# Kernel optimization log

Measured on AMD Instinct MI355X. Metric: run time of the kernel, lower is better.

The kernel has to match this reference:

```python
import jax, jax.numpy as jnp
import numpy as np

DIM = 768
D_STATE = 16
D_INNER = 2 * DIM  # expand=2


def setup_inputs() -> dict:
    key = jax.random.key(0)
    k_x, k_in, k_conv, k_out = jax.random.split(key, 4)
    B, L = 1, 4096
    x = jax.random.normal(k_x, (B, L, DIM), dtype=jnp.float32)
    # torch Linear weight layout: [out_features, in_features]
    W_in = jax.random.normal(k_in, (3 * D_INNER + 2 * D_STATE, DIM), dtype=jnp.float32) * 0.02
    # depthwise conv1d kernel: [out_ch=d_inner, in_ch/groups=1, k=3]
    W_conv = jax.random.normal(k_conv, (D_INNER, 1, 3), dtype=jnp.float32) * 0.1
    W_out = jax.random.normal(k_out, (DIM, D_INNER), dtype=jnp.float32) * 0.02
    A_log = jnp.log(jnp.tile(jnp.arange(1, D_STATE + 1, dtype=jnp.float32), (D_INNER, 1)))
    D = jnp.ones((D_INNER,), dtype=jnp.float32)
    return {"x": x, "W_in": W_in, "W_conv": W_conv, "W_out": W_out, "A_log": A_log, "D": D}


def reference(x, W_in, W_conv, W_out, A_log, D):
    d_inner = W_conv.shape[0]
    d_state = A_log.shape[1]
    Bsz = x.shape[0]

    xz = x @ W_in.T  # [B, L, 3*d_inner + 2*d_state]
    x_inner, z, B_ssm, C_ssm, delta = jnp.split(
        xz, [d_inner, 2 * d_inner, 2 * d_inner + d_state, 2 * d_inner + 2 * d_state], axis=-1
    )

    # depthwise conv over sequence: [B, d_inner, L]
    xc = jax.lax.conv_general_dilated(
        x_inner.transpose(0, 2, 1), W_conv,
        window_strides=(1,), padding=[(1, 1)], feature_group_count=d_inner,
    ).transpose(0, 2, 1)  # back to [B, L, d_inner]
    xc = jax.nn.silu(xc)

    A = -jnp.exp(A_log)  # [d_inner, d_state]
    delta = jax.nn.softplus(delta)  # [B, L, d_inner]
    dA = jnp.exp(jnp.einsum('bld,dn->bldn', delta, A))           # [B, L, d_inner, d_state]
    dBx = jnp.einsum('bld,bln,bld->bldn', delta, B_ssm, xc)      # delta_B * x fused

    def step(h, inp):
        da_t, dbx_t, c_t = inp  # [B,d,n], [B,d,n], [B,n]
        h = da_t * h + dbx_t
        y_t = jnp.einsum('bdn,bn->bd', h, c_t)
        return h, y_t

    h0 = jnp.zeros((Bsz, d_inner, d_state), dtype=x.dtype)
    _, ys = jax.lax.scan(
        step, h0,
        (dA.transpose(1, 0, 2, 3), dBx.transpose(1, 0, 2, 3), C_ssm.transpose(1, 0, 2)),
    )  # ys: [L, B, d_inner]

    y = ys.transpose(1, 0, 2) + xc * D  # skip connection
    y = y * jax.nn.silu(z)
    return y @ W_out.T  # [B, L, dim]
```

## Files before the change

### kernel.cpp

```cpp
#include <hip/hip_runtime.h>
#include <hip/hip_bf16.h>
#include <math.h>

#define LSEQ   4096
#define DIM    768
#define DINNER 1536
#define DSTATE 16
#define NCOLS  4640
#define NCH    128
#define CLEN   32
#define NPAD   4736
#define DXW    1568

typedef _Float16 f16;
typedef __attribute__((ext_vector_type(8))) _Float16 f16x8;
typedef __attribute__((ext_vector_type(4))) float f32x4;

__device__ __forceinline__ void gld_lds16(void* lds_dst, const void* gsrc) {
    __builtin_amdgcn_global_load_lds(
        (__attribute__((address_space(1))) void*)(gsrc),
        (__attribute__((address_space(3))) void*)(lds_dst), 16, 0, 0);
}

#define G1K    768
#define G1_NT  12
#define G1_BM  256
#define G1_BN  128
#define G1_RT  384
#define G1_LDSE (G1_RT * 64)

__global__ __launch_bounds__(512) void gemm1_pipe(const f16* __restrict__ A,
                                                  const f16* __restrict__ B,
                                                  float* __restrict__ C,
                                                  f16* __restrict__ Xb,
                                                  f16* __restrict__ Zb) {
    __shared__ __align__(16) f16 S[3 * G1_LDSE];

    const int P   = gridDim.x >> 3;
    const int idx = (blockIdx.x & 7) * P + (blockIdx.x >> 3);
    const int m0  = (idx & 15) * G1_BM;
    const int n0  = (idx >> 4) * G1_BN;

    const int tid  = threadIdx.x;
    const int w    = tid >> 6;
    const int lane = tid & 63;
    const int wr   = w >> 1;
    const int wc   = w & 1;
    const int m    = lane & 15;
    const int q    = lane >> 4;
    const int rl8  = lane >> 3;
    const int bsel = lane & 7;

    const f16* gb[6];
#pragma unroll
    for (int s = 0; s < 6; ++s) {
        const int rl  = (w + 8 * s) * 8 + rl8;
        const int blk = bsel ^ (rl & 7);
        gb[s] = (rl < G1_BM) ? A + (size_t)(m0 + rl) * G1K + blk * 8
                             : B + (size_t)(n0 + rl - G1_BM) * G1K + blk * 8;
    }

    f32x4 acc[4][4];
#pragma unroll
    for (int i = 0; i < 4; i++)
#pragma unroll
        for (int j = 0; j < 4; j++) acc[i][j] = (f32x4){0.f, 0.f, 0.f, 0.f};

    auto stg2 = [&](int kt, int s0) {
        f16* dst = S + (kt % 3) * G1_LDSE;
#pragma unroll
        for (int s = s0; s < s0 + 2; ++s)
            gld_lds16(dst + (w + 8 * s) * 512, gb[s] + kt * 64);
    };
    auto stg6 = [&](int kt) {
        f16* dst = S + (kt % 3) * G1_LDSE;
#pragma unroll
        for (int s = 0; s < 6; ++s)
            gld_lds16(dst + (w + 8 * s) * 512, gb[s] + kt * 64);
    };

    stg6(0);
    stg6(1);

#pragma unroll
    for (int kt = 0; kt < G1_NT; ++kt) {
        if (kt < G1_NT - 1) asm volatile("s_waitcnt vmcnt(6)" ::: "memory");
        else                asm volatile("s_waitcnt vmcnt(0)" ::: "memory");
        __builtin_amdgcn_s_barrier();
        const f16* As = S + (kt % 3) * G1_LDSE;
        const f16* Bs = As + G1_BM * 64;
        const bool pf = (kt + 2 < G1_NT);

        f16x8 af0[2][2], af2[2][2], bh0[2][2], bh2[2][2];

#pragma unroll
        for (int kk = 0; kk < 2; ++kk) {
            const int fo = (((q + 4 * kk) ^ (m & 7)) << 3);
#pragma unroll
            for (int i = 0; i < 2; ++i) {
                af0[kk][i] = *(const f16x8*)&As[(wr * 64 + i * 16 + m) * 64 + fo];
                bh0[kk][i] = *(const f16x8*)&Bs[(wc * 64 + i * 16 + m) * 64 + fo];
            }
        }
        if (pf) stg2(kt + 2, 0);
        __builtin_amdgcn_s_barrier();
        asm volatile("s_waitcnt lgkmcnt(0)" ::: "memory");
        __builtin_amdgcn_sched_barrier(0);
        __builtin_amdgcn_s_setprio(1);
#pragma unroll
        for (int kk = 0; kk < 2; ++kk)
#pragma unroll
            for (int i = 0; i < 2; ++i)
#pragma unroll
                for (int j = 0; j < 2; ++j)
                    acc[i][j] = __builtin_amdgcn_mfma_f32_16x16x32_f16(
                        af0[kk][i], bh0[kk][j], acc[i][j], 0, 0, 0);
        __builtin_amdgcn_s_setprio(0);

#pragma unroll
        for (int kk = 0; kk < 2; ++kk) {
            const int fo = (((q + 4 * kk) ^ (m & 7)) << 3);
#pragma unroll
            for (int j = 0; j < 2; ++j)
                bh2[kk][j] = *(const f16x8*)&Bs[(wc * 64 + (j + 2) * 16 + m) * 64 + fo];
        }
        if (pf) stg2(kt + 2, 2);
        __builtin_amdgcn_s_barrier();
        asm volatile("s_waitcnt lgkmcnt(0)" ::: "memory");
        __builtin_amdgcn_sched_barrier(0);
        __builtin_amdgcn_s_setprio(1);
#pragma unroll
        for (int kk = 0; kk < 2; ++kk)
#pragma unroll
            for (int i = 0; i < 2; ++i)
#pragma unroll
                for (int j = 0; j < 2; ++j)
                    acc[i][j + 2] = __builtin_amdgcn_mfma_f32_16x16x32_f16(
                        af0[kk][i], bh2[kk][j], acc[i][j + 2], 0, 0, 0);
        __builtin_amdgcn_s_setprio(0);

#pragma unroll
        for (int kk = 0; kk < 2; ++kk) {
            const int fo = (((q + 4 * kk) ^ (m & 7)) << 3);
#pragma unroll
            for (int i = 0; i < 2; ++i)
                af2[kk][i] = *(const f16x8*)&As[(wr * 64 + (i + 2) * 16 + m) * 64 + fo];
        }
        if (pf) stg2(kt + 2, 4);
        __builtin_amdgcn_s_barrier();
        asm volatile("s_waitcnt lgkmcnt(0)" ::: "memory");
        __builtin_amdgcn_sched_barrier(0);
        __builtin_amdgcn_s_setprio(1);
#pragma unroll
        for (int kk = 0; kk < 2; ++kk)
#pragma unroll
            for (int i = 0; i < 2; ++i)
#pragma unroll
                for (int j = 0; j < 2; ++j)
                    acc[i + 2][j] = __builtin_amdgcn_mfma_f32_16x16x32_f16(
                        af2[kk][i], bh0[kk][j], acc[i + 2][j], 0, 0, 0);
        __builtin_amdgcn_s_setprio(0);

        __builtin_amdgcn_s_setprio(1);
#pragma unroll
        for (int kk = 0; kk < 2; ++kk)
#pragma unroll
            for (int i = 0; i < 2; ++i)
#pragma unroll
                for (int j = 0; j < 2; ++j)
                    acc[i + 2][j + 2] = __builtin_amdgcn_mfma_f32_16x16x32_f16(
                        af2[kk][i], bh2[kk][j], acc[i + 2][j + 2], 0, 0, 0);
        __builtin_amdgcn_s_setprio(0);
    }

    if (n0 < DINNER) {
#pragma unroll
        for (int i = 0; i < 4; i++)
#pragma unroll
            for (int j = 0; j < 4; j++) {
                const int col  = n0 + wc * 64 + j * 16 + m;
                const int rowb = m0 + wr * 64 + i * 16 + q * 4;
#pragma unroll
                for (int r = 0; r < 4; r++)
                    Xb[(size_t)(rowb + r) * DINNER + col] = (f16)acc[i][j][r];
            }
        return;
    }
    if (n0 < 2 * DINNER) {
#pragma unroll
        for (int i = 0; i < 4; i++)
#pragma unroll
            for (int j = 0; j < 4; j++) {
                const int col  = n0 - DINNER + wc * 64 + j * 16 + m;
                const int rowb = m0 + wr * 64 + i * 16 + q * 4;
#pragma unroll
                for (int r = 0; r < 4; r++)
                    Zb[(size_t)(rowb + r) * DINNER + col] = (f16)acc[i][j][r];
            }
        return;
    }
#pragma unroll
    for (int i = 0; i < 4; i++)
#pragma unroll
        for (int j = 0; j < 4; j++) {
            const int col = n0 - 2 * DINNER + wc * 64 + j * 16 + m;
            if (col >= DXW) continue;
            const int rowb = m0 + wr * 64 + i * 16 + q * 4;
#pragma unroll
            for (int r = 0; r < 4; r++)
                C[(size_t)(rowb + r) * DXW + col] = acc[i][j][r];
        }
}

template<int BM, int BN, int WM, int WN, int NTB, bool COLM, bool ZMODE>
__global__ __launch_bounds__(256) void gemm_f16(const f16* __restrict__ A,
                                                const f16* __restrict__ B,
                                                float* __restrict__ C,
                                                f16* __restrict__ Xb,
                                                f16* __restrict__ Zb,
                                                int M, int N, int K, int ldc) {
    constexpr int MI  = WM / 16;
    constexpr int NI  = WN / 16;
    constexpr int NWN = BN / WN;
    constexpr int RT  = BM + BN;
    constexpr int NS  = RT / 8;

    __shared__ __align__(16) f16 S[RT * 64];
    f16* As = S;
    f16* Bs = S + BM * 64;

    const int P   = gridDim.x >> 3;
    const int idx = (blockIdx.x & 7) * P + (blockIdx.x >> 3);
    const int m0  = (COLM ? (idx % NTB) : (idx / NTB)) * BM;
    const int n0  = (COLM ? (idx / NTB) : (idx % NTB)) * BN;

    const int tid  = threadIdx.x;
    const int w    = tid >> 6;
    const int lane = tid & 63;
    const int wr   = w / NWN;
    const int wc   = w % NWN;
    const int m    = lane & 15;
    const int q    = lane >> 4;
    const int rl8  = lane >> 3;
    const int bsel = lane & 7;

    f32x4 acc[MI][NI];
#pragma unroll
    for (int i = 0; i < MI; i++)
#pragma unroll
        for (int j = 0; j < NI; j++) acc[i][j] = (f32x4){0.f, 0.f, 0.f, 0.f};

    for (int k0 = 0; k0 < K; k0 += 64) {
#pragma unroll
        for (int t = w; t < NS; t += 4) {
            const int rl  = t * 8 + rl8;
            const int blk = bsel ^ (rl & 7);
            const f16* g = (rl < BM)
                ? A + (size_t)(m0 + rl) * K + k0 + blk * 8
                : B + (size_t)(n0 + rl - BM) * K + k0 + blk * 8;
            gld_lds16(S + t * 8 * 64, g);
        }
        __syncthreads();

#pragma unroll
        for (int kk = 0; kk < 2; kk++) {
            const int fo = (((q + 4 * kk) ^ (m & 7)) << 3);
            f16x8 af[MI], bh[NI];
#pragma unroll
            for (int i = 0; i < MI; i++)
                af[i] = *(const f16x8*)&As[(wr * WM + i * 16 + m) * 64 + fo];
#pragma unroll
            for (int j = 0; j < NI; j++)
                bh[j] = *(const f16x8*)&Bs[(wc * WN + j * 16 + m) * 64 + fo];
#pragma unroll
            for (int i = 0; i < MI; i++)
#pragma unroll
                for (int j = 0; j < NI; j++)
                    acc[i][j] = __builtin_amdgcn_mfma_f32_16x16x32_f16(
                        af[i], bh[j], acc[i][j], 0, 0, 0);
        }
        __syncthreads();
    }

    if (ZMODE && n0 < DINNER) {
#pragma unroll
        for (int i = 0; i < MI; i++)
#pragma unroll
            for (int j = 0; j < NI; j++) {
                const int col  = n0 + wc * WN + j * 16 + m;
                const int rowb = m0 + wr * WM + i * 16 + q * 4;
#pragma unroll
                for (int r = 0; r < 4; r++)
                    Xb[(size_t)(rowb + r) * DINNER + col] = (f16)acc[i][j][r];
            }
        return;
    }
    if (ZMODE && n0 < 2 * DINNER) {
#pragma unroll
        for (int i = 0; i < MI; i++)
#pragma unroll
            for (int j = 0; j < NI; j++) {
                const int col  = n0 - DINNER + wc * WN + j * 16 + m;
                const int rowb = m0 + wr * WM + i * 16 + q * 4;
#pragma unroll
                for (int r = 0; r < 4; r++)
                    Zb[(size_t)(rowb + r) * DINNER + col] = (f16)acc[i][j][r];
            }
        return;
    }
#pragma unroll
    for (int i = 0; i < MI; i++)
#pragma unroll
        for (int j = 0; j < NI; j++) {
            const int col  = (ZMODE ? n0 - 2 * DINNER : n0) + wc * WN + j * 16 + m;
            const int lim  = ZMODE ? DXW : N;
            if (col >= lim) continue;
            const int rowb = m0 + wr * WM + i * 16 + q * 4;
#pragma unroll
            for (int r = 0; r < 4; r++)
                C[(size_t)(rowb + r) * ldc + col] = acc[i][j][r];
        }
}

#define E0 (LSEQ * DIM)
#define E1 (E0 + NPAD * DIM)
#define E2 (E1 + DIM * DINNER)

__global__ __launch_bounds__(256) void cvt_all(const float* __restrict__ x,
                                               const float* __restrict__ Wi,
                                               const float* __restrict__ Wo,
                                               f16* __restrict__ Ax,
                                               f16* __restrict__ Bw,
                                               f16* __restrict__ Bo) {
    int i = (blockIdx.x * 256 + threadIdx.x) * 4;
    if (i < E0) {
        float4 v = *(const float4*)(x + i);
        Ax[i] = (f16)v.x; Ax[i+1] = (f16)v.y; Ax[i+2] = (f16)v.z; Ax[i+3] = (f16)v.w;
    } else if (i < E1) {
        int e = i - E0;
        int n = e / DIM;
        if (n < NCOLS) {
            float4 v = *(const float4*)(Wi + e);
            Bw[e] = (f16)v.x; Bw[e+1] = (f16)v.y; Bw[e+2] = (f16)v.z; Bw[e+3] = (f16)v.w;
        } else {
            Bw[e] = (f16)0.f; Bw[e+1] = (f16)0.f; Bw[e+2] = (f16)0.f; Bw[e+3] = (f16)0.f;
        }
    } else if (i < E2) {
        int e = i - E1;
        float4 v = *(const float4*)(Wo + e);
        Bo[e] = (f16)v.x; Bo[e+1] = (f16)v.y; Bo[e+2] = (f16)v.z; Bo[e+3] = (f16)v.w;
    }
}

__global__ __launch_bounds__(256) void scan1_kernel(const float* __restrict__ Dxz,
                                                    const f16* __restrict__ Xb,
                                                    const float* __restrict__ Wc,
                                                    const float* __restrict__ A_log,
                                                    float* __restrict__ aprod,
                                                    float* __restrict__ hend) {
    __shared__ float Bs[CLEN * DSTATE];
    const int d  = blockIdx.x * 256 + threadIdx.x;
    const int c  = blockIdx.y;
    const int l0 = c * CLEN;
    for (int i = threadIdx.x; i < CLEN * DSTATE; i += 256)
        Bs[i] = Dxz[(size_t)(l0 + (i >> 4)) * DXW + (i & 15)];
    float Areg[DSTATE];
#pragma unroll
    for (int n = 0; n < DSTATE; n++) Areg[n] = -__expf(A_log[d * DSTATE + n]);
    const float w0 = Wc[d * 3 + 0], w1 = Wc[d * 3 + 1], w2 = Wc[d * 3 + 2];
    float xm = (l0 > 0) ? (float)Xb[(size_t)(l0 - 1) * DINNER + d] : 0.f;
    float x0 = (float)Xb[(size_t)l0 * DINNER + d];
    float ld_xp   = (float)Xb[(size_t)(l0 + 1) * DINNER + d];
    float ld_draw = Dxz[(size_t)l0 * DXW + 32 + d];
    __syncthreads();

    float h[DSTATE];
#pragma unroll
    for (int n = 0; n < DSTATE; n++) h[n] = 0.f;
    float S = 0.f;

    for (int t = 0; t < CLEN; t++) {
        const int l = l0 + t;
        float xp = ld_xp, draw = ld_draw;
        if (t + 1 < CLEN) {
            ld_xp   = (l + 2 < LSEQ) ? (float)Xb[(size_t)(l + 2) * DINNER + d] : 0.f;
            ld_draw = Dxz[(size_t)(l + 1) * DXW + 32 + d];
        }
        float v  = xm * w0 + x0 * w1 + xp * w2;
        float xcv = __fdividef(v, 1.f + __expf(-v));
        float dtv = (draw > 20.f) ? draw : __logf(1.f + __expf(draw));
        float u = dtv * xcv;
        S += dtv;
#pragma unroll
        for (int n = 0; n < DSTATE; n++) {
            float e = __expf(dtv * Areg[n]);
            h[n] = e * h[n] + u * Bs[t * DSTATE + n];
        }
        xm = x0; x0 = xp;
    }
#pragma unroll
    for (int n = 0; n < DSTATE; n++) {
        size_t idx = ((size_t)c * DSTATE + n) * DINNER + d;
        aprod[idx] = __expf(S * Areg[n]);
        hend[idx]  = h[n];
    }
}

__global__ __launch_bounds__(256) void scan2_kernel(const float* __restrict__ aprod,
                                                    const float* __restrict__ hend,
                                                    float* __restrict__ hinit) {
    const int g = blockIdx.x * 256 + threadIdx.x;
    const size_t S = (size_t)DSTATE * DINNER;
    size_t idx = g;
    float a = aprod[idx], e = hend[idx];
    float h = 0.f;
#pragma unroll 4
    for (int c = 0; c < NCH; c++) {
        float ac = a, ec = e;
        if (c + 1 < NCH) { a = aprod[idx + S]; e = hend[idx + S]; }
        hinit[idx] = h;
        h = ac * h + ec;
        idx += S;
    }
}

__global__ __launch_bounds__(256) void scan3_kernel(const float* __restrict__ Dxz,
                                                    const f16* __restrict__ Xb,
                                                    const f16* __restrict__ Zb,
                                                    const float* __restrict__ Wc,
                                                    const float* __restrict__ A_log,
                                                    const float* __restrict__ hinit,
                                                    const float* __restrict__ Dp,
                                                    f16* __restrict__ Ay) {
    __shared__ float Bs[CLEN * DSTATE];
    __shared__ float Cs[CLEN * DSTATE];
    const int d  = blockIdx.x * 256 + threadIdx.x;
    const int c  = blockIdx.y;
    const int l0 = c * CLEN;
    for (int i = threadIdx.x; i < CLEN * DSTATE; i += 256) {
        size_t roff = (size_t)(l0 + (i >> 4)) * DXW;
        Bs[i] = Dxz[roff + (i & 15)];
        Cs[i] = Dxz[roff + 16 + (i & 15)];
    }
    float Areg[DSTATE];
#pragma unroll
    for (int n = 0; n < DSTATE; n++) Areg[n] = -__expf(A_log[d * DSTATE + n]);
    float h[DSTATE];
#pragma unroll
    for (int n = 0; n < DSTATE; n++)
        h[n] = hinit[((size_t)c * DSTATE + n) * DINNER + d];
    const float Dv = Dp[d];
    const float w0 = Wc[d * 3 + 0], w1 = Wc[d * 3 + 1], w2 = Wc[d * 3 + 2];
    float xm = (l0 > 0) ? (float)Xb[(size_t)(l0 - 1) * DINNER + d] : 0.f;
    float x0 = (float)Xb[(size_t)l0 * DINNER + d];
    float ld_xp   = (float)Xb[(size_t)(l0 + 1) * DINNER + d];
    float ld_draw = Dxz[(size_t)l0 * DXW + 32 + d];
    float ld_z    = (float)Zb[(size_t)l0 * DINNER + d];
    __syncthreads();

    for (int t = 0; t < CLEN; t++) {
        const int l = l0 + t;
        float xp = ld_xp, draw = ld_draw, zv = ld_z;
        if (t + 1 < CLEN) {
            ld_xp   = (l + 2 < LSEQ) ? (float)Xb[(size_t)(l + 2) * DINNER + d] : 0.f;
            ld_draw = Dxz[(size_t)(l + 1) * DXW + 32 + d];
            ld_z    = (float)Zb[(size_t)(l + 1) * DINNER + d];
        }
        float v  = xm * w0 + x0 * w1 + xp * w2;
        float xcv = __fdividef(v, 1.f + __expf(-v));
        float dtv = (draw > 20.f) ? draw : __logf(1.f + __expf(draw));
        float u = dtv * xcv;
        float y = 0.f;
#pragma unroll
        for (int n = 0; n < DSTATE; n++) {
            float e = __expf(dtv * Areg[n]);
            h[n] = e * h[n] + u * Bs[t * DSTATE + n];
            y += h[n] * Cs[t * DSTATE + n];
        }
        float sz = __fdividef(zv, 1.f + __expf(-zv));
        Ay[(size_t)l * DINNER + d] = (f16)((y + xcv * Dv) * sz);
        xm = x0; x0 = xp;
    }
}

extern "C" void kernel_launch(void* const* d_in, const int* in_sizes, int n_in,
                              void* d_out, int out_size, void* d_ws, size_t ws_size,
                              hipStream_t stream) {
    const float* x     = (const float*)d_in[0];
    const float* W_in  = (const float*)d_in[1];
    const float* W_conv= (const float*)d_in[2];
    const float* W_out = (const float*)d_in[3];
    const float* A_log = (const float*)d_in[4];
    const float* Dp    = (const float*)d_in[5];
    float* out = (float*)d_out;

    float* ws  = (float*)d_ws;
    float* Dxz = ws;
    float* ap  = Dxz + (size_t)LSEQ * DXW;
    float* he  = ap + (size_t)NCH * DSTATE * DINNER;
    float* hi  = he + (size_t)NCH * DSTATE * DINNER;
    f16* Ax = (f16*)(hi + (size_t)NCH * DSTATE * DINNER);
    f16* Ay = Ax + (size_t)LSEQ * DIM;
    f16* Bw = Ay + (size_t)LSEQ * DINNER;
    f16* Bo = Bw + (size_t)NPAD * DIM;
    f16* Zb = Bo + (size_t)DIM * DINNER;
    f16* Xb = Zb + (size_t)LSEQ * DINNER;

    cvt_all<<<E2 / 1024, 256, 0, stream>>>(x, W_in, W_out, Ax, Bw, Bo);

    gemm1_pipe<<<592, 512, 0, stream>>>(Ax, Bw, Dxz, Xb, Zb);

    scan1_kernel<<<dim3(DINNER / 256, NCH), 256, 0, stream>>>(
        Dxz, Xb, W_conv, A_log, ap, he);
    scan2_kernel<<<(DINNER * DSTATE) / 256, 256, 0, stream>>>(ap, he, hi);
    scan3_kernel<<<dim3(DINNER / 256, NCH), 256, 0, stream>>>(
        Dxz, Xb, Zb, W_conv, A_log, hi, Dp, Ay);

    gemm_f16<64, 64, 32, 32, 12, false, false><<<768, 256, 0, stream>>>(
        Ay, Bo, out, nullptr, nullptr, LSEQ, DIM, DINNER, DIM);
}
```

Before: 240.0 us.

## Halve scan chunk length, prefetch deeper in carry scan, reuse aprod buffer in place

Doubles the number of scan chunks (chunk length 32 to 16) so scan1 and scan3 launch twice as many blocks with shorter sequential loops. The carry-propagation kernel now batch-prefetches eight chunks' worth of aprod/hend values in two register groups to hide load latency. It also writes the initial states in place over the aprod buffer, dropping the separate hinit allocation. The cost is twice the chunk-state traffic and a longer sequential pass in scan2.

```diff
diff --git a/kernel.cpp b/kernel.cpp
--- a/kernel.cpp
+++ b/kernel.cpp
@@ -7,8 +7,8 @@
 #define DINNER 1536
 #define DSTATE 16
 #define NCOLS  4640
-#define NCH    128
-#define CLEN   32
+#define NCH    256
+#define CLEN   16
 #define NPAD   4736
 #define DXW    1568
 
@@ -406,21 +406,40 @@
     }
 }
 
-__global__ __launch_bounds__(256) void scan2_kernel(const float* __restrict__ aprod,
-                                                    const float* __restrict__ hend,
-                                                    float* __restrict__ hinit) {
+__global__ __launch_bounds__(256) void scan2_kernel(float* __restrict__ aphi,
+                                                    const float* __restrict__ hend) {
     const int g = blockIdx.x * 256 + threadIdx.x;
     const size_t S = (size_t)DSTATE * DINNER;
-    size_t idx = g;
-    float a = aprod[idx], e = hend[idx];
+    float aA[4], eA[4], aB[4], eB[4];
+#pragma unroll
+    for (int k = 0; k < 4; ++k) {
+        aA[k] = aphi[g + (size_t)k * S];
+        eA[k] = hend[g + (size_t)k * S];
+    }
     float h = 0.f;
-#pragma unroll 4
-    for (int c = 0; c < NCH; c++) {
-        float ac = a, ec = e;
-        if (c + 1 < NCH) { a = aprod[idx + S]; e = hend[idx + S]; }
-        hinit[idx] = h;
-        h = ac * h + ec;
-        idx += S;
+    for (int c = 0; c < NCH; c += 8) {
+#pragma unroll
+        for (int k = 0; k < 4; ++k) {
+            aB[k] = aphi[g + (size_t)(c + 4 + k) * S];
+            eB[k] = hend[g + (size_t)(c + 4 + k) * S];
+        }
+#pragma unroll
+        for (int k = 0; k < 4; ++k) {
+            aphi[g + (size_t)(c + k) * S] = h;
+            h = aA[k] * h + eA[k];
+        }
+        if (c + 8 < NCH) {
+#pragma unroll
+            for (int k = 0; k < 4; ++k) {
+                aA[k] = aphi[g + (size_t)(c + 8 + k) * S];
+                eA[k] = hend[g + (size_t)(c + 8 + k) * S];
+            }
+        }
+#pragma unroll
+        for (int k = 0; k < 4; ++k) {
+            aphi[g + (size_t)(c + 4 + k) * S] = h;
+            h = aB[k] * h + eB[k];
+        }
     }
 }
 
@@ -498,8 +517,7 @@
     float* Dxz = ws;
     float* ap  = Dxz + (size_t)LSEQ * DXW;
     float* he  = ap + (size_t)NCH * DSTATE * DINNER;
-    float* hi  = he + (size_t)NCH * DSTATE * DINNER;
-    f16* Ax = (f16*)(hi + (size_t)NCH * DSTATE * DINNER);
+    f16* Ax = (f16*)(he + (size_t)NCH * DSTATE * DINNER);
     f16* Ay = Ax + (size_t)LSEQ * DIM;
     f16* Bw = Ay + (size_t)LSEQ * DINNER;
     f16* Bo = Bw + (size_t)NPAD * DIM;
@@ -512,9 +530,9 @@
 
     scan1_kernel<<<dim3(DINNER / 256, NCH), 256, 0, stream>>>(
         Dxz, Xb, W_conv, A_log, ap, he);
-    scan2_kernel<<<(DINNER * DSTATE) / 256, 256, 0, stream>>>(ap, he, hi);
+    scan2_kernel<<<(DINNER * DSTATE) / 256, 256, 0, stream>>>(ap, he);
     scan3_kernel<<<dim3(DINNER / 256, NCH), 256, 0, stream>>>(
-        Dxz, Xb, Zb, W_conv, A_log, hi, Dp, Ay);
+        Dxz, Xb, Zb, W_conv, A_log, ap, Dp, Ay);
 
     gemm_f16<64, 64, 32, 32, 12, false, false><<<768, 256, 0, stream>>>(
         Ay, Bo, out, nullptr, nullptr, LSEQ, DIM, DINNER, DIM);
```

Result: slower. 247.8 us (+3.2%).
